# Kernel tuning notes

Measured on AMD Instinct MI355X. Metric: run time of the kernel, lower is better.

The kernel has to match this reference:

```python
import jax, jax.numpy as jnp
import numpy as np

B, C, D, H, W = 4, 128, 16, 16, 16
C8 = C // 8
TEXT = 256
N = D * H * W


def setup_inputs() -> dict:
    key = jax.random.key(0)
    ks = jax.random.split(key, 13)
    s = lambda fan: 1.0 / np.sqrt(fan)
    return {
        "x": jax.random.normal(ks[0], (B, C, D, H, W), jnp.float32),
        "text_emb": jax.random.normal(ks[1], (B, TEXT), jnp.float32),
        "Wq": jax.random.normal(ks[2], (C8, C), jnp.float32) * s(C),
        "bq": jax.random.normal(ks[3], (C8,), jnp.float32) * 0.01,
        "Wk": jax.random.normal(ks[4], (C8, C), jnp.float32) * s(C),
        "bk": jax.random.normal(ks[5], (C8,), jnp.float32) * 0.01,
        "Wv": jax.random.normal(ks[6], (C, C), jnp.float32) * s(C),
        "bv": jax.random.normal(ks[7], (C,), jnp.float32) * 0.01,
        "Wtk": jax.random.normal(ks[8], (C8, TEXT), jnp.float32) * s(TEXT),
        "btk": jax.random.normal(ks[9], (C8,), jnp.float32) * 0.01,
        "Wtv": jax.random.normal(ks[10], (C, TEXT), jnp.float32) * s(TEXT),
        "btv": jax.random.normal(ks[11], (C,), jnp.float32) * 0.01,
        # gamma is zero-init in the original; use a nonzero value so the
        # attention path contributes to the output (and to gradients).
        "gamma": jax.random.normal(ks[12], (1,), jnp.float32) * 0.1 + 0.5,
    }


def reference(x, text_emb, Wq, bq, Wk, bk, Wv, bv, Wtk, btk, Wtv, btv, gamma):
    b, c, d, h, w = x.shape
    n = d * h * w
    xf = x.reshape(b, c, n)                       # [B, C, N]
    # 1x1x1 convs == channel matmuls
    q = jnp.einsum('oc,bcn->bno', Wq, xf) + bq    # [B, N, C8]
    k = jnp.einsum('oc,bcn->bon', Wk, xf) + bk[None, :, None]  # [B, C8, N]
    v = jnp.einsum('oc,bcn->bon', Wv, xf) + bv[None, :, None]  # [B, C, N]
    # text-conditioned additive key/value (broadcast over all voxels)
    tk = (text_emb @ Wtk.T + btk)[:, :, None]     # [B, C8, 1]
    tv = (text_emb @ Wtv.T + btv)[:, :, None]     # [B, C, 1]
    k = k + tk
    v = v + tv
    # unscaled attention: softmax over keys
    scores = jnp.einsum('bno,bom->bnm', q, k)     # [B, N, N]
    attn = jax.nn.softmax(scores, axis=-1)
    # out[b,c,n] = sum_m v[b,c,m] * attn[b,n,m]
    out = jnp.einsum('bcm,bnm->bcn', v, attn).reshape(b, c, d, h, w)
    return gamma * out + x
```

## Files before the change

### kernel.cpp

```cpp
#include <hip/hip_runtime.h>
#include <math.h>

#define BB 4
#define CC 128
#define C8 16
#define TEXTN 256
#define NN 4096
#define WQB 64
#define NT 32

typedef __attribute__((ext_vector_type(8))) __bf16 bf16x8;
typedef __attribute__((ext_vector_type(16))) float f32x16;

#define LOG2E 1.44269504088896340736f

static __device__ __forceinline__ ushort f2bf(float f) {
  unsigned u = __builtin_bit_cast(unsigned, f);
  u += 0x7FFFu + ((u >> 16) & 1u);
  return (ushort)(u >> 16);
}

static __device__ __forceinline__ float exp2a(float x) {
#if __has_builtin(__builtin_amdgcn_exp2f)
  return __builtin_amdgcn_exp2f(x);
#else
  return exp2f(x);
#endif
}

static __device__ __forceinline__ unsigned cvt_pk_bf16(float lo, float hi) {
  unsigned r;
  asm("v_cvt_pk_bf16_f32 %0, %1, %2" : "=v"(r) : "v"(lo), "v"(hi));
  return r;
}
static __device__ __forceinline__ void pl32swap(unsigned &a, unsigned &b) {
  asm("v_permlane32_swap_b32 %0, %1" : "+v"(a), "+v"(b));
}

__global__ __launch_bounds__(256) void k_text(
    const float* __restrict__ text, const float* __restrict__ Wtk,
    const float* __restrict__ btk, const float* __restrict__ Wtv,
    const float* __restrict__ btv, float* __restrict__ tkv) {
  __shared__ float ts[TEXTN];
  int b = blockIdx.x;
  for (int i = threadIdx.x; i < TEXTN; i += 256) ts[i] = text[b * TEXTN + i];
  __syncthreads();
  int o = threadIdx.x;
  if (o < 144) {
    const float* w;
    float acc;
    if (o < 16) { w = Wtk + o * TEXTN; acc = btk[o]; }
    else        { w = Wtv + (o - 16) * TEXTN; acc = btv[o - 16]; }
    #pragma unroll 8
    for (int t = 0; t < TEXTN; t++) acc += w[t] * ts[t];
    tkv[b * 144 + o] = acc;
  }
}

__global__ __launch_bounds__(320) void k_qkv(
    const float* __restrict__ x,
    const float* __restrict__ Wq, const float* __restrict__ bq,
    const float* __restrict__ Wk, const float* __restrict__ bk,
    const float* __restrict__ Wv, const float* __restrict__ bv,
    const float* __restrict__ tkv,
    ushort* __restrict__ qt, ushort* __restrict__ kt, ushort* __restrict__ vtB) {
  __shared__ __align__(16) ushort xs[64 * 128];
  int b = blockIdx.x >> 6;
  int n0 = (blockIdx.x & 63) * 64;
  int t = threadIdx.x;
  int w = t >> 6, lane = t & 63, l31 = lane & 31, hi = lane >> 5;

  for (int i = t; i < 1024; i += 320) {
    int n = i & 63, ch = i >> 6;
    union { ushort u[8]; uint4 v; } pk;
    #pragma unroll
    for (int j = 0; j < 8; ++j)
      pk.u[j] = f2bf(x[((size_t)b * CC + ch * 8 + j) * NN + n0 + n]);
    *(uint4*)&xs[n * 128 + ((ch ^ (n & 15)) << 3)] = pk.v;
  }

  const float* wrow;
  if (w == 0) wrow = (l31 < 16) ? (Wq + l31 * CC) : (Wk + (l31 - 16) * CC);
  else        wrow = Wv + (size_t)(32 * (w - 1) + l31) * CC;
  bf16x8 af[8];
  #pragma unroll
  for (int ks = 0; ks < 8; ++ks) {
    float4 u0 = *(const float4*)&wrow[ks * 16 + hi * 8];
    float4 u1 = *(const float4*)&wrow[ks * 16 + hi * 8 + 4];
    union { ushort u[8]; bf16x8 v; } tmp;
    tmp.u[0] = f2bf(u0.x); tmp.u[1] = f2bf(u0.y); tmp.u[2] = f2bf(u0.z); tmp.u[3] = f2bf(u0.w);
    tmp.u[4] = f2bf(u1.x); tmp.u[5] = f2bf(u1.y); tmp.u[6] = f2bf(u1.z); tmp.u[7] = f2bf(u1.w);
    af[ks] = tmp.v;
  }
  float badd[16];
  #pragma unroll
  for (int r = 0; r < 16; ++r) {
    int ol = (r & 3) + 8 * (r >> 2) + 4 * hi;
    if (w == 0) badd[r] = (ol < 16) ? bq[ol] : (bk[ol - 16] + tkv[b * 144 + ol - 16]);
    else { int c = 32 * (w - 1) + ol; badd[r] = bv[c] + tkv[b * 144 + 16 + c]; }
  }
  __syncthreads();

  #pragma unroll
  for (int n32 = 0; n32 < 2; ++n32) {
    int n = n32 * 32 + l31;
    int ng = n0 + n;
    bf16x8 bf[8];
    #pragma unroll
    for (int ks = 0; ks < 8; ++ks)
      bf[ks] = *(const bf16x8*)&xs[n * 128 + (((ks * 2 + hi) ^ (n & 15)) << 3)];
    f32x16 d;
    #pragma unroll
    for (int r = 0; r < 16; ++r) d[r] = 0.f;
    #pragma unroll
    for (int ks = 0; ks < 8; ++ks)
      d = __builtin_amdgcn_mfma_f32_32x32x16_bf16(af[ks], bf[ks], d, 0, 0, 0);
    #pragma unroll
    for (int g = 0; g < 4; ++g) {
      int o0 = 8 * g + 4 * hi;
      float v0 = d[g * 4 + 0] + badd[g * 4 + 0];
      float v1 = d[g * 4 + 1] + badd[g * 4 + 1];
      float v2 = d[g * 4 + 2] + badd[g * 4 + 2];
      float v3 = d[g * 4 + 3] + badd[g * 4 + 3];
      if (w == 0 && o0 < 16) { v0 *= LOG2E; v1 *= LOG2E; v2 *= LOG2E; v3 *= LOG2E; }
      ushort4 pkv;
      pkv.x = f2bf(v0); pkv.y = f2bf(v1); pkv.z = f2bf(v2); pkv.w = f2bf(v3);
      if (w == 0) {
        if (o0 < 16) *(ushort4*)&qt[(b * NN + ng) * C8 + o0] = pkv;
        else         *(ushort4*)&kt[(b * NN + ng) * C8 + o0 - 16] = pkv;
      } else {
        int c0 = 32 * (w - 1) + o0;
        int base = b * (NN / 8) * CC * 8 + (ng >> 3) * (CC * 8) + (ng & 7);
        vtB[base + (c0 + 0) * 8] = pkv.x;
        vtB[base + (c0 + 1) * 8] = pkv.y;
        vtB[base + (c0 + 2) * 8] = pkv.z;
        vtB[base + (c0 + 3) * 8] = pkv.w;
      }
    }
  }
}

__global__ __launch_bounds__(512) void k_attn(
    const ushort* __restrict__ qt, const ushort* __restrict__ kt,
    const ushort* __restrict__ vtB, const float* __restrict__ x,
    const float* __restrict__ gamma_p, float* __restrict__ out) {
  __shared__ __align__(16) float mergeAcc[4][2][1024];
  __shared__ float mergeL[4][2][2][32];
  __shared__ float invGL[64];

  int raw = blockIdx.x;
  int xcd = raw & 7, slot = raw >> 3;
  int b = xcd >> 1;
  int q0 = ((xcd & 1) * 32 + slot) * WQB;

  int t = threadIdx.x;
  int w = t >> 6, lane = t & 63, l31 = lane & 31, hi = lane >> 5;
  int ms = w >> 1, ch = w & 1;

  const ushort* ktb = kt + (size_t)b * NN * C8;
  const ushort* vbb = vtB + (size_t)b * (NN / 8) * CC * 8;

  bf16x8 qfA = *(const bf16x8*)&qt[((size_t)b * NN + q0 + l31) * C8 + hi * 8];
  bf16x8 qfB = *(const bf16x8*)&qt[((size_t)b * NN + q0 + 32 + l31) * C8 + hi * 8];

  f32x16 accA0, accA1, accB0, accB1;
  #pragma unroll
  for (int r = 0; r < 16; ++r) { accA0[r] = 0.f; accA1[r] = 0.f; accB0[r] = 0.f; accB1[r] = 0.f; }
  float lpA = 0.f, lpB = 0.f;

  f32x16 z;
  #pragma unroll
  for (int r = 0; r < 16; ++r) z[r] = 0.f;

  const ushort* kp  = ktb + (ms * 32 + l31) * C8 + hi * 8;
  const ushort* vp0 = vbb + (size_t)(ms * 4 + 0 + hi) * (CC * 8) + (ch * 64 + l31) * 8;
  const ushort* vp1 = vbb + (size_t)(ms * 4 + 2 + hi) * (CC * 8) + (ch * 64 + l31) * 8;

  bf16x8 kfA, kfB;
  kfA = *(const bf16x8*)kp; kp += 128 * C8;

#define MKPF(P, OUT0, OUT1)                                                   \
  {                                                                           \
    unsigned a0 = cvt_pk_bf16(P[0], P[1]), b0 = cvt_pk_bf16(P[4], P[5]);      \
    unsigned c0 = cvt_pk_bf16(P[2], P[3]), d0 = cvt_pk_bf16(P[6], P[7]);      \
    pl32swap(a0, b0); pl32swap(c0, d0);                                       \
    union { unsigned u[4]; bf16x8 v; } u0; u0.u[0] = a0; u0.u[1] = c0;        \
    u0.u[2] = b0; u0.u[3] = d0; OUT0 = u0.v;                                  \
    unsigned a1 = cvt_pk_bf16(P[8], P[9]), b1 = cvt_pk_bf16(P[12], P[13]);    \
    unsigned c1 = cvt_pk_bf16(P[10], P[11]), d1 = cvt_pk_bf16(P[14], P[15]);  \
    pl32swap(a1, b1); pl32swap(c1, d1);                                       \
    union { unsigned u[4]; bf16x8 v; } u1; u1.u[0] = a1; u1.u[1] = c1;        \
    u1.u[2] = b1; u1.u[3] = d1; OUT1 = u1.v;                                  \
  }

#define STEP(CK, NK)                                                          \
  {                                                                           \
    NK = *(const bf16x8*)kp; kp += 128 * C8;                                  \
    bf16x8 vA0 = *(const bf16x8*)(vp0);                   \
    bf16x8 vA1 = *(const bf16x8*)(vp0 + 256);             \
    bf16x8 vB0 = *(const bf16x8*)(vp1);                   \
    bf16x8 vB1 = *(const bf16x8*)(vp1 + 256);             \
    vp0 += 16 * CC * 8; vp1 += 16 * CC * 8;                                   \
    f32x16 sA = __builtin_amdgcn_mfma_f32_32x32x16_bf16(CK, qfA, z, 0, 0, 0); \
    f32x16 sB = __builtin_amdgcn_mfma_f32_32x32x16_bf16(CK, qfB, z, 0, 0, 0); \
    float pA[16], pB[16];                                                     \
    _Pragma("unroll")                                                         \
    for (int r = 0; r < 16; ++r) pA[r] = exp2a(sA[r]);                        \
    _Pragma("unroll")                                                         \
    for (int r = 0; r < 16; ++r) pB[r] = exp2a(sB[r]);                        \
    {                                                                         \
      float y0 = (pA[0] + pA[1]) + (pA[2] + pA[3]);                           \
      float y1 = (pA[4] + pA[5]) + (pA[6] + pA[7]);                           \
      float y2 = (pA[8] + pA[9]) + (pA[10] + pA[11]);                         \
      float y3 = (pA[12] + pA[13]) + (pA[14] + pA[15]);                       \
      lpA += (y0 + y1) + (y2 + y3);                                           \
      float u0 = (pB[0] + pB[1]) + (pB[2] + pB[3]);                           \
      float u1 = (pB[4] + pB[5]) + (pB[6] + pB[7]);                           \
      float u2 = (pB[8] + pB[9]) + (pB[10] + pB[11]);                         \
      float u3 = (pB[12] + pB[13]) + (pB[14] + pB[15]);                       \
      lpB += (u0 + u1) + (u2 + u3);                                           \
    }                                                                         \
    bf16x8 pfA0, pfA1, pfB0, pfB1;                                            \
    MKPF(pA, pfA0, pfA1)                                                      \
    MKPF(pB, pfB0, pfB1)                                                      \
    __builtin_amdgcn_s_setprio(1);                                            \
    accA0 = __builtin_amdgcn_mfma_f32_32x32x16_bf16(vA0, pfA0, accA0, 0, 0, 0); \
    accA1 = __builtin_amdgcn_mfma_f32_32x32x16_bf16(vA1, pfA0, accA1, 0, 0, 0); \
    accB0 = __builtin_amdgcn_mfma_f32_32x32x16_bf16(vA0, pfB0, accB0, 0, 0, 0); \
    accB1 = __builtin_amdgcn_mfma_f32_32x32x16_bf16(vA1, pfB0, accB1, 0, 0, 0); \
    accA0 = __builtin_amdgcn_mfma_f32_32x32x16_bf16(vB0, pfA1, accA0, 0, 0, 0); \
    accA1 = __builtin_amdgcn_mfma_f32_32x32x16_bf16(vB1, pfA1, accA1, 0, 0, 0); \
    accB0 = __builtin_amdgcn_mfma_f32_32x32x16_bf16(vB0, pfB1, accB0, 0, 0, 0); \
    accB1 = __builtin_amdgcn_mfma_f32_32x32x16_bf16(vB1, pfB1, accB1, 0, 0, 0); \
    __builtin_amdgcn_s_setprio(0);                                            \
  }

  for (int tt = 0; tt < NT; tt += 2) {
    STEP(kfA, kfB)
    STEP(kfB, kfA)
  }
#undef STEP
#undef MKPF

  if (ch == 0) {
    mergeL[ms][hi][0][l31] = lpA;
    mergeL[ms][hi][1][l31] = lpB;
  }
  __syncthreads();
  if (t < 64) {
    float L = 0.f;
    #pragma unroll
    for (int m2 = 0; m2 < 4; ++m2)
      #pragma unroll
      for (int h2 = 0; h2 < 2; ++h2) L += mergeL[m2][h2][t >> 5][t & 31];
    invGL[t] = gamma_p[0] / L;
  }

#define EPI(ACC, QT, CB, FIRST)                                               \
  {                                                                           \
    if (!(FIRST)) __syncthreads();                                            \
    _Pragma("unroll")                                                         \
    for (int r = 0; r < 16; ++r)                                              \
      mergeAcc[ms][ch][(((r & 3) + 8 * (r >> 2) + 4 * hi) << 5) | l31] = ACC[r]; \
    __syncthreads();                                                          \
    int idx = t * 4;                                                          \
    int qq = idx & 31, cl = idx >> 5;                                         \
    int chh = cl >> 5, crow = cl & 31;                                        \
    float4 sum = *(const float4*)&mergeAcc[0][chh][crow * 32 + qq];           \
    _Pragma("unroll")                                                         \
    for (int m2 = 1; m2 < 4; ++m2) {                                          \
      float4 sv = *(const float4*)&mergeAcc[m2][chh][crow * 32 + qq];         \
      sum.x += sv.x; sum.y += sv.y; sum.z += sv.z; sum.w += sv.w;             \
    }                                                                         \
    float4 gl = *(const float4*)&invGL[(QT) * 32 + qq];                       \
    int c = chh * 64 + (CB) * 32 + crow;                                      \
    size_t base = ((size_t)b * CC + c) * NN + q0 + (QT) * 32 + qq;            \
    float4 xv = *(const float4*)&x[base];                                     \
    float4 ov;                                                                \
    ov.x = sum.x * gl.x + xv.x;                                               \
    ov.y = sum.y * gl.y + xv.y;                                               \
    ov.z = sum.z * gl.z + xv.z;                                               \
    ov.w = sum.w * gl.w + xv.w;                                               \
    *(float4*)&out[base] = ov;                                                \
  }

  EPI(accA0, 0, 0, 1)
  EPI(accA1, 0, 1, 0)
  EPI(accB0, 1, 0, 0)
  EPI(accB1, 1, 1, 0)
#undef EPI
}

extern "C" void kernel_launch(void* const* d_in, const int* in_sizes, int n_in,
                              void* d_out, int out_size, void* d_ws, size_t ws_size,
                              hipStream_t stream) {
  const float* x     = (const float*)d_in[0];
  const float* text  = (const float*)d_in[1];
  const float* Wq    = (const float*)d_in[2];
  const float* bq    = (const float*)d_in[3];
  const float* Wk    = (const float*)d_in[4];
  const float* bk    = (const float*)d_in[5];
  const float* Wv    = (const float*)d_in[6];
  const float* bv    = (const float*)d_in[7];
  const float* Wtk   = (const float*)d_in[8];
  const float* btk   = (const float*)d_in[9];
  const float* Wtv   = (const float*)d_in[10];
  const float* btv   = (const float*)d_in[11];
  const float* gamma = (const float*)d_in[12];
  float* outp = (float*)d_out;

  char* wsb = (char*)d_ws;
  float*  tkv = (float*)wsb;
  ushort* qt  = (ushort*)(wsb + 4096);
  ushort* kt  = (ushort*)(wsb + 4096 + 524288);
  ushort* vtB = (ushort*)(wsb + 4096 + 2 * 524288);

  k_text<<<BB, 256, 0, stream>>>(text, Wtk, btk, Wtv, btv, tkv);
  k_qkv<<<BB * NN / 64, 320, 0, stream>>>(x, Wq, bq, Wk, bk, Wv, bv, tkv, qt, kt, vtB);
  k_attn<<<BB * (NN / WQB), 512, 0, stream>>>(qt, kt, vtB, x, gamma, outp);
}
```

Baseline: 51.73 us.

## Software-pipeline QK exp with previous tile's PV MFMAs

Restructures the attention inner loop into a two-stage software pipeline. Each step issues the QK MFMA for tile t, then the PV MFMAs for tile t-1 using already-packed probabilities, then exp/pack for tile t. A prologue and epilogue are added, with even/odd register sets for V and P. This lets the exp work overlap with the matrix-core work instead of serializing behind it, at the cost of higher register pressure.

```diff
diff --git a/kernel.cpp b/kernel.cpp
--- a/kernel.cpp
+++ b/kernel.cpp
@@ -177,7 +177,10 @@
   const ushort* vp1 = vbb + (size_t)(ms * 4 + 2 + hi) * (CC * 8) + (ch * 64 + l31) * 8;
 
   bf16x8 kfA, kfB;
-  kfA = *(const bf16x8*)kp; kp += 128 * C8;
+  bf16x8 vE0, vE1, vE2, vE3;
+  bf16x8 vO0, vO1, vO2, vO3;
+  bf16x8 paE0, paE1, pbE0, pbE1;
+  bf16x8 paO0, paO1, pbO0, pbO1;
 
 #define MKPF(P, OUT0, OUT1)                                                   \
   {                                                                           \
@@ -193,21 +196,20 @@
     u1.u[2] = b1; u1.u[3] = d1; OUT1 = u1.v;                                  \
   }
 
-#define STEP(CK, NK)                                                          \
-  {                                                                           \
-    NK = *(const bf16x8*)kp; kp += 128 * C8;                                  \
-    bf16x8 vA0 = *(const bf16x8*)(vp0);                   \
-    bf16x8 vA1 = *(const bf16x8*)(vp0 + 256);             \
-    bf16x8 vB0 = *(const bf16x8*)(vp1);                   \
-    bf16x8 vB1 = *(const bf16x8*)(vp1 + 256);             \
-    vp0 += 16 * CC * 8; vp1 += 16 * CC * 8;                                   \
-    f32x16 sA = __builtin_amdgcn_mfma_f32_32x32x16_bf16(CK, qfA, z, 0, 0, 0); \
-    f32x16 sB = __builtin_amdgcn_mfma_f32_32x32x16_bf16(CK, qfB, z, 0, 0, 0); \
+#define LOADV(L0, L1, L2, L3)                                                 \
+    L0 = *(const bf16x8*)(vp0); L1 = *(const bf16x8*)(vp0 + 256);             \
+    L2 = *(const bf16x8*)(vp1); L3 = *(const bf16x8*)(vp1 + 256);             \
+    vp0 += 16 * CC * 8; vp1 += 16 * CC * 8;
+
+#define EXPPACK(SA, SB, PA0, PA1, PB0, PB1)                                   \
+  {                                                                           \
     float pA[16], pB[16];                                                     \
     _Pragma("unroll")                                                         \
-    for (int r = 0; r < 16; ++r) pA[r] = exp2a(sA[r]);                        \
+    for (int r = 0; r < 16; ++r) pA[r] = exp2a(SA[r]);                        \
     _Pragma("unroll")                                                         \
-    for (int r = 0; r < 16; ++r) pB[r] = exp2a(sB[r]);                        \
+    for (int r = 0; r < 16; ++r) pB[r] = exp2a(SB[r]);                        \
+    MKPF(pA, PA0, PA1)                                                        \
+    MKPF(pB, PB0, PB1)                                                        \
     {                                                                         \
       float y0 = (pA[0] + pA[1]) + (pA[2] + pA[3]);                           \
       float y1 = (pA[4] + pA[5]) + (pA[6] + pA[7]);                           \
@@ -220,26 +222,58 @@
       float u3 = (pB[12] + pB[13]) + (pB[14] + pB[15]);                       \
       lpB += (u0 + u1) + (u2 + u3);                                           \
     }                                                                         \
-    bf16x8 pfA0, pfA1, pfB0, pfB1;                                            \
-    MKPF(pA, pfA0, pfA1)                                                      \
-    MKPF(pB, pfB0, pfB1)                                                      \
+  }
+
+#define PVSTEP(V0, V1, V2, V3, UA0, UA1, UB0, UB1)                            \
+  {                                                                           \
     __builtin_amdgcn_s_setprio(1);                                            \
-    accA0 = __builtin_amdgcn_mfma_f32_32x32x16_bf16(vA0, pfA0, accA0, 0, 0, 0); \
-    accA1 = __builtin_amdgcn_mfma_f32_32x32x16_bf16(vA1, pfA0, accA1, 0, 0, 0); \
-    accB0 = __builtin_amdgcn_mfma_f32_32x32x16_bf16(vA0, pfB0, accB0, 0, 0, 0); \
-    accB1 = __builtin_amdgcn_mfma_f32_32x32x16_bf16(vA1, pfB0, accB1, 0, 0, 0); \
-    accA0 = __builtin_amdgcn_mfma_f32_32x32x16_bf16(vB0, pfA1, accA0, 0, 0, 0); \
-    accA1 = __builtin_amdgcn_mfma_f32_32x32x16_bf16(vB1, pfA1, accA1, 0, 0, 0); \
-    accB0 = __builtin_amdgcn_mfma_f32_32x32x16_bf16(vB0, pfB1, accB0, 0, 0, 0); \
-    accB1 = __builtin_amdgcn_mfma_f32_32x32x16_bf16(vB1, pfB1, accB1, 0, 0, 0); \
+    accA0 = __builtin_amdgcn_mfma_f32_32x32x16_bf16(V0, UA0, accA0, 0, 0, 0); \
+    accA1 = __builtin_amdgcn_mfma_f32_32x32x16_bf16(V1, UA0, accA1, 0, 0, 0); \
+    accB0 = __builtin_amdgcn_mfma_f32_32x32x16_bf16(V0, UB0, accB0, 0, 0, 0); \
+    accB1 = __builtin_amdgcn_mfma_f32_32x32x16_bf16(V1, UB0, accB1, 0, 0, 0); \
+    accA0 = __builtin_amdgcn_mfma_f32_32x32x16_bf16(V2, UA1, accA0, 0, 0, 0); \
+    accA1 = __builtin_amdgcn_mfma_f32_32x32x16_bf16(V3, UA1, accA1, 0, 0, 0); \
+    accB0 = __builtin_amdgcn_mfma_f32_32x32x16_bf16(V2, UB1, accB0, 0, 0, 0); \
+    accB1 = __builtin_amdgcn_mfma_f32_32x32x16_bf16(V3, UB1, accB1, 0, 0, 0); \
     __builtin_amdgcn_s_setprio(0);                                            \
   }
 
-  for (int tt = 0; tt < NT; tt += 2) {
-    STEP(kfA, kfB)
-    STEP(kfB, kfA)
-  }
+#define STEP(KC, KN, VL0,VL1,VL2,VL3, VU0,VU1,VU2,VU3,                        \
+             UA0,UA1,UB0,UB1, PA0,PA1,PB0,PB1)                                \
+  {                                                                           \
+    LOADV(VL0, VL1, VL2, VL3)                                                 \
+    KN = *(const bf16x8*)kp; kp += 128 * C8;                                  \
+    f32x16 sA = __builtin_amdgcn_mfma_f32_32x32x16_bf16(KC, qfA, z, 0, 0, 0); \
+    f32x16 sB = __builtin_amdgcn_mfma_f32_32x32x16_bf16(KC, qfB, z, 0, 0, 0); \
+    PVSTEP(VU0, VU1, VU2, VU3, UA0, UA1, UB0, UB1)                            \
+    EXPPACK(sA, sB, PA0, PA1, PB0, PB1)                                       \
+  }
+
+  kfA = *(const bf16x8*)kp; kp += 128 * C8;
+  LOADV(vE0, vE1, vE2, vE3)
+  kfB = *(const bf16x8*)kp; kp += 128 * C8;
+  {
+    f32x16 sA = __builtin_amdgcn_mfma_f32_32x32x16_bf16(kfA, qfA, z, 0, 0, 0);
+    f32x16 sB = __builtin_amdgcn_mfma_f32_32x32x16_bf16(kfA, qfB, z, 0, 0, 0);
+    EXPPACK(sA, sB, paE0, paE1, pbE0, pbE1)
+  }
+
+  for (int tt = 1; tt <= 29; tt += 2) {
+    STEP(kfB, kfA, vO0,vO1,vO2,vO3, vE0,vE1,vE2,vE3,
+         paE0,paE1,pbE0,pbE1, paO0,paO1,pbO0,pbO1)
+    STEP(kfA, kfB, vE0,vE1,vE2,vE3, vO0,vO1,vO2,vO3,
+         paO0,paO1,pbO0,pbO1, paE0,paE1,pbE0,pbE1)
+  }
+
+  STEP(kfB, kfA, vO0,vO1,vO2,vO3, vE0,vE1,vE2,vE3,
+       paE0,paE1,pbE0,pbE1, paO0,paO1,pbO0,pbO1)
+
+  PVSTEP(vO0, vO1, vO2, vO3, paO0, paO1, pbO0, pbO1)
+
 #undef STEP
+#undef PVSTEP
+#undef EXPPACK
+#undef LOADV
 #undef MKPF
 
   if (ch == 0) {
```

Measured after the change: 50.97 us. About the same (-1.5%).
